# Optimization experiments

Hardware: AMD Instinct MI355X
Metric: run time of the kernel (lower is better)

The kernel has to match this reference:

```python
import jax, jax.numpy as jnp
import numpy as np

DEPTH = 6
N_LEAF = 2 ** DEPTH          # 64
GATE_COUNT = N_LEAF - 1      # 63
B = 1024
GATING_FEATURES = 512
IN_FEATURES = 512
OUT_FEATURES = 512


def setup_inputs() -> dict:
    key = jax.random.key(0)
    k1, k2, k3, k4 = jax.random.split(key, 4)
    x_gating = jax.random.normal(k1, (B, GATING_FEATURES), dtype=jnp.float32)
    x_leaf = jax.random.normal(k2, (B, IN_FEATURES), dtype=jnp.float32)
    # kaiming-normal-ish init scales
    gw = jax.random.normal(k3, (GATING_FEATURES, GATE_COUNT), dtype=jnp.float32) * (1.0 / np.sqrt(GATING_FEATURES))
    gb = jnp.zeros((GATE_COUNT,), dtype=jnp.float32)
    pw = jax.random.normal(k4, (OUT_FEATURES, IN_FEATURES, N_LEAF), dtype=jnp.float32) * (1.0 / np.sqrt(IN_FEATURES))
    pb = jnp.zeros((OUT_FEATURES, N_LEAF), dtype=jnp.float32)
    return {"x_gating": x_gating, "x_leaf": x_leaf, "gw": gw, "gb": gb, "pw": pw, "pb": pb}


def _leaf_probs(x_gating, gw, gb):
    # gatings: (B, gate_count), internal nodes in breadth-first order
    gatings = jax.nn.sigmoid(x_gating @ gw + gb)
    b = gatings.shape[0]
    dens = jnp.ones((b, 1), dtype=gatings.dtype)  # root density
    start = 0
    for d in range(DEPTH):
        n_par = 2 ** d
        g = gatings[:, start:start + n_par]          # (B, n_par)
        # left child (even it+1) gets g, right child gets 1-g, interleaved
        dens = jnp.stack([dens * g, dens * (1.0 - g)], axis=-1).reshape(b, 2 * n_par)
        start += n_par
    return dens  # (B, n_leaf) = leaf densities (last n_leaf node densities)


def reference(x_gating, x_leaf, gw, gb, pw, pb):
    leaf_probs = _leaf_probs(x_gating, gw, gb)              # (B, L)
    # gated projection applied to x_leaf, summed over leaves:
    # equals ((pw @ leaf_probs.T).permute(2,0,1) @ x_leaf[...,None])[...,0]
    result = jnp.einsum('oil,bl,bi->bo', pw, leaf_probs, x_leaf)
    result = result + leaf_probs @ pb.T                     # gated bias (B, O)
    return result
```

## Files before the change

kernel.cpp:

```cpp
#include <hip/hip_runtime.h>
#include <stdint.h>

#define B_SZ   1024
#define GF     512
#define GC     63
#define NLEAF  64
#define IN_F   512
#define OUT_F  512

typedef float f32x4 __attribute__((ext_vector_type(4)));
typedef __fp16 h16x2 __attribute__((ext_vector_type(2)));
typedef __fp16 h16x8 __attribute__((ext_vector_type(8)));
typedef _Float16 f16x2 __attribute__((ext_vector_type(2)));

union HF8 { f16x2 h2[4]; h16x8 v; uint4 u; };

__device__ inline f16x2 pkrtz(float a, float b) {
  union { h16x2 r; f16x2 f; } u;
  u.r = __builtin_amdgcn_cvt_pkrtz(a, b);
  return u.f;
}

__global__ __launch_bounds__(512, 2) void k_leafprobs(
    const float* __restrict__ xg, const float* __restrict__ gw,
    const float* __restrict__ gb, float* __restrict__ p_ws)
{
  __shared__ float xsr[GF];
  __shared__ float part[512];
  __shared__ float gates[GC + 1];
  const int b = blockIdx.x;
  const int t = threadIdx.x;

  xsr[t] = xg[(size_t)b * GF + t];
  __syncthreads();

  const int ks = t >> 6, g = t & 63;
  float acc = 0.f;
  if (g < GC) {
    const float* gp = gw + (size_t)(ks * 64) * GC + g;
    const float* xp = &xsr[ks * 64];
#pragma unroll 8
    for (int k = 0; k < 64; ++k) acc += xp[k] * gp[(size_t)k * GC];
  }
  part[t] = acc;
  __syncthreads();

  if (t < GC) {
    float s = gb[t];
#pragma unroll
    for (int r = 0; r < 8; ++r) s += part[r * 64 + t];
    gates[t] = 1.f / (1.f + expf(-s));
  }
  __syncthreads();

  if (t < NLEAF) {
    float v = 1.f;
    int idx = 0, start = 0;
#pragma unroll
    for (int d = 0; d < 6; ++d) {
      int bit = (t >> (5 - d)) & 1;
      float gg = gates[start + idx];
      v *= bit ? (1.f - gg) : gg;
      idx = 2 * idx + bit;
      start += (1 << d);
    }
    p_ws[(size_t)b * NLEAF + t] = v;
  }
}

#define SK 16
#define KI 32

template <bool ATOMIC>
__global__ __launch_bounds__(256, 2) void k_fused(
    const float* __restrict__ x_leaf,
    const float* __restrict__ p_ws,
    const float* __restrict__ pw,
    float* __restrict__ dst)
{
  __shared__ __align__(16) float         xs[KI][256];
  __shared__ __align__(16) unsigned char bs8[2 * 8192];

  const int tid  = threadIdx.x;
  const int lane = tid & 63;
  const int wid  = tid >> 6;
  const int quad = lane >> 4;
  const int l15  = lane & 15;
  const int l7   = l15 & 7;

  const int bid = blockIdx.x;
  const int nt  = bid & 7;
  const int mt  = (bid >> 3) & 3;
  const int kc  = bid >> 5;

  const int row_m0 = mt * 256;
  const int o0     = nt * 64;
  const int i0     = kc * KI;
  const int wm     = wid * 64;

  {
    const float* src = x_leaf + (size_t)(row_m0 + tid) * IN_F + i0;
#pragma unroll
    for (int q = 0; q < 8; ++q) {
      float4 v = *(const float4*)(src + q * 4);
      xs[q * 4 + 0][tid] = v.x;
      xs[q * 4 + 1][tid] = v.y;
      xs[q * 4 + 2][tid] = v.z;
      xs[q * 4 + 3][tid] = v.w;
    }
  }

  HF8 prh[4][2];
#pragma unroll
  for (int mi = 0; mi < 4; ++mi) {
    const int row = row_m0 + wm + mi * 16 + l15;
#pragma unroll
    for (int ks = 0; ks < 2; ++ks) {
      const f32x4* src = (const f32x4*)(p_ws + (size_t)row * NLEAF + ks * 32 + quad * 8);
      f32x4 lo = src[0], hi = src[1];
      prh[mi][ks].h2[0] = pkrtz(lo.x, lo.y);
      prh[mi][ks].h2[1] = pkrtz(lo.z, lo.w);
      prh[mi][ks].h2[2] = pkrtz(hi.x, hi.y);
      prh[mi][ks].h2[3] = pkrtz(hi.z, hi.w);
    }
  }

  const int br  = tid >> 2;
  const int seg = tid & 3;
  const float* bsrc0 = pw + ((size_t)(o0 + br) * IN_F + i0) * NLEAF + seg * 16;

  const int wsw   = (br & 7) << 4;
  const int woff0 = br * 128 + ((seg * 32) ^ wsw);
  const int woff1 = br * 128 + ((seg * 32 + 16) ^ wsw);
  int coff[2];
#pragma unroll
  for (int ks = 0; ks < 2; ++ks)
    coff[ks] = (ks * 64 + quad * 16) ^ (l7 << 4);
  const int rbase = l15 * 128;

  f32x4 acc[4][4];
#pragma unroll
  for (int mi = 0; mi < 4; ++mi)
#pragma unroll
    for (int ni = 0; ni < 4; ++ni)
      acc[mi][ni] = (f32x4)(0.f);

  float4 rb[4][4];

#define BLOAD(T, SLOT)                                                        \
  {                                                                           \
    const float4* s_ = (const float4*)(bsrc0 + (size_t)(T) * NLEAF);          \
    rb[SLOT][0] = s_[0]; rb[SLOT][1] = s_[1];                                 \
    rb[SLOT][2] = s_[2]; rb[SLOT][3] = s_[3];                                 \
  }

#define BSTAGE(SLOT, BUF)                                                     \
  {                                                                           \
    HF8 c0_, c1_;                                                             \
    float4 a0_ = rb[SLOT][0], a1_ = rb[SLOT][1];                              \
    float4 a2_ = rb[SLOT][2], a3_ = rb[SLOT][3];                              \
    c0_.h2[0] = pkrtz(a0_.x, a0_.y);                                          \
    c0_.h2[1] = pkrtz(a0_.z, a0_.w);                                          \
    c0_.h2[2] = pkrtz(a1_.x, a1_.y);                                          \
    c0_.h2[3] = pkrtz(a1_.z, a1_.w);                                          \
    c1_.h2[0] = pkrtz(a2_.x, a2_.y);                                          \
    c1_.h2[1] = pkrtz(a2_.z, a2_.w);                                          \
    c1_.h2[2] = pkrtz(a3_.x, a3_.y);                                          \
    c1_.h2[3] = pkrtz(a3_.z, a3_.w);                                          \
    *(uint4*)(bs8 + (BUF) * 8192 + woff0) = c0_.u;                            \
    *(uint4*)(bs8 + (BUF) * 8192 + woff1) = c1_.u;                            \
  }

#define BARRIER() asm volatile("s_waitcnt lgkmcnt(0)\n\ts_barrier" ::: "memory")

#define STEP(IT, BUF, SNX)                                                    \
  {                                                                           \
    float xvf[4];                                                             \
    _Float16 xh[4];                                                           \
    _Pragma("unroll")                                                         \
    for (int mi = 0; mi < 4; ++mi) xvf[mi] = xs[(IT)][wm + mi * 16 + l15];    \
    _Pragma("unroll")                                                         \
    for (int mi = 0; mi < 4; ++mi) xh[mi] = (_Float16)xvf[mi];                \
    const unsigned char* bsr_ = bs8 + (BUF) * 8192;                           \
    __builtin_amdgcn_s_setprio(1);                                            \
    _Pragma("unroll")                                                         \
    for (int ks = 0; ks < 2; ++ks) {                                          \
      h16x8 af[4];                                                            \
      _Pragma("unroll")                                                       \
      for (int mi = 0; mi < 4; ++mi) {                                        \
        HF8 t_;                                                               \
        f16x2 xp_; xp_[0] = xh[mi]; xp_[1] = xh[mi];                          \
        _Pragma("unroll")                                                     \
        for (int j = 0; j < 4; ++j) t_.h2[j] = prh[mi][ks].h2[j] * xp_;       \
        af[mi] = t_.v;                                                        \
      }                                                                       \
      _Pragma("unroll")                                                       \
      for (int ni = 0; ni < 4; ++ni) {                                        \
        h16x8 bfr = *(const h16x8*)(bsr_ + ni * 2048 + rbase + coff[ks]);     \
        _Pragma("unroll")                                                     \
        for (int mi = 0; mi < 4; ++mi)                                        \
          acc[mi][ni] = __builtin_amdgcn_mfma_f32_16x16x32_f16(               \
              af[mi], bfr, acc[mi][ni], 0, 0, 0);                             \
      }                                                                       \
    }                                                                         \
    __builtin_amdgcn_s_setprio(0);                                            \
    if ((IT) + 1 < KI) { BSTAGE(SNX, (BUF) ^ 1) }                             \
    if ((IT) + 5 < KI) { BLOAD((IT) + 5, SNX) }                               \
    BARRIER();                                                                \
  }

  BLOAD(0, 0)
  BLOAD(1, 1)
  BLOAD(2, 2)
  BLOAD(3, 3)
  BSTAGE(0, 0)
  BLOAD(4, 0)
  BARRIER();

  for (int itb = 0; itb < KI; itb += 4) {
    STEP(itb + 0, 0, 1)
    STEP(itb + 1, 1, 2)
    STEP(itb + 2, 0, 3)
    STEP(itb + 3, 1, 0)
  }
#undef BLOAD
#undef BSTAGE
#undef BARRIER
#undef STEP

#pragma unroll
  for (int mi = 0; mi < 4; ++mi) {
#pragma unroll
    for (int ni = 0; ni < 4; ++ni) {
      int row = row_m0 + wm + mi * 16 + quad * 4;
      int col = o0 + ni * 16 + l15;
      if (ATOMIC) {
        float* o = dst + (size_t)row * OUT_F + col;
        atomicAdd(o,             acc[mi][ni][0]);
        atomicAdd(o + OUT_F,     acc[mi][ni][1]);
        atomicAdd(o + 2 * OUT_F, acc[mi][ni][2]);
        atomicAdd(o + 3 * OUT_F, acc[mi][ni][3]);
      } else {
        float* o = dst + ((size_t)kc << 19) + (size_t)row * OUT_F + col;
        o[0]         = acc[mi][ni][0];
        o[OUT_F]     = acc[mi][ni][1];
        o[2 * OUT_F] = acc[mi][ni][2];
        o[3 * OUT_F] = acc[mi][ni][3];
      }
    }
  }
}

__global__ __launch_bounds__(256, 4) void k_reduce(
    const float* __restrict__ parts, const float* __restrict__ p_ws,
    const float* __restrict__ pb, float* __restrict__ out, int nparts)
{
  __shared__ float ps_l[2 * NLEAF];
  const int t  = threadIdx.x;
  const int b0 = blockIdx.x * 2;

  if (t < 32)
    ((f32x4*)ps_l)[t] = ((const f32x4*)(p_ws + (size_t)b0 * NLEAF))[t];
  __syncthreads();

  const int row = b0 + (t >> 7);
  const int c0  = (t & 127) * 4;
  const f32x4* ps = (const f32x4*)&ps_l[(t >> 7) * NLEAF];

  f32x4 a;
#pragma unroll
  for (int jo = 0; jo < 4; ++jo) {
    const f32x4* pbo = (const f32x4*)(pb + (size_t)(c0 + jo) * NLEAF);
    f32x4 s = (f32x4)(0.f);
#pragma unroll
    for (int lv = 0; lv < 16; ++lv) s += pbo[lv] * ps[lv];
    a[jo] = s.x + s.y + s.z + s.w;
  }

#pragma unroll 8
  for (int k = 0; k < nparts; ++k)
    a += *(const f32x4*)(parts + ((size_t)k << 19) + (size_t)row * OUT_F + c0);

  *(f32x4*)(out + (size_t)row * OUT_F + c0) = a;
}

extern "C" void kernel_launch(void* const* d_in, const int* in_sizes, int n_in,
                              void* d_out, int out_size, void* d_ws, size_t ws_size,
                              hipStream_t stream) {
  const float* xg = (const float*)d_in[0];
  const float* xl = (const float*)d_in[1];
  const float* gw = (const float*)d_in[2];
  const float* gb = (const float*)d_in[3];
  const float* pw = (const float*)d_in[4];
  const float* pb = (const float*)d_in[5];
  float* out = (float*)d_out;

  const size_t P_BYTES = (size_t)B_SZ * NLEAF * 4;
  const size_t SLICE   = (size_t)B_SZ * OUT_F * 4;

  float* p_ws  = (float*)d_ws;
  float* parts = (float*)((char*)d_ws + P_BYTES);

  k_leafprobs<<<dim3(B_SZ), dim3(512), 0, stream>>>(xg, gw, gb, p_ws);

  if (ws_size >= P_BYTES + SK * SLICE) {
    k_fused<false><<<dim3(512), dim3(256), 0, stream>>>(xl, p_ws, pw, parts);
    k_reduce<<<dim3(512), dim3(256), 0, stream>>>(parts, p_ws, pb, out, SK);
  } else {
    k_reduce<<<dim3(512), dim3(256), 0, stream>>>(parts, p_ws, pb, out, 0);
    k_fused<true><<<dim3(512), dim3(256), 0, stream>>>(xl, p_ws, pw, out);
  }
}
```

Baseline: 167.4 us.

## Load weight fragments directly into registers, dropping LDS staging and per-step barriers

The pw operand for the MFMA is no longer staged through shared memory. Each lane now loads its own B fragment straight from global memory with inline-asm dwordx4 loads, using a one-step register prefetch and explicit vmcnt waits, so the LDS stores, LDS reads and per-iteration barriers go away. The cost is that each wave loads its 64x64 weight tile independently, so the four waves in a block load the same data four times. The prefetch is also shallower than the previous four-slot register ring, so global latency is less hidden.

```diff
diff --git a/kernel.cpp b/kernel.cpp
--- a/kernel.cpp
+++ b/kernel.cpp
@@ -78,15 +78,13 @@
     const float* __restrict__ pw,
     float* __restrict__ dst)
 {
-  __shared__ __align__(16) float         xs[KI][256];
-  __shared__ __align__(16) unsigned char bs8[2 * 8192];
+  __shared__ __align__(16) float xs[KI][256];
 
   const int tid  = threadIdx.x;
   const int lane = tid & 63;
   const int wid  = tid >> 6;
   const int quad = lane >> 4;
   const int l15  = lane & 15;
-  const int l7   = l15 & 7;
 
   const int bid = blockIdx.x;
   const int nt  = bid & 7;
@@ -109,6 +107,7 @@
       xs[q * 4 + 3][tid] = v.w;
     }
   }
+  __syncthreads();
 
   HF8 prh[4][2];
 #pragma unroll
@@ -118,25 +117,17 @@
     for (int ks = 0; ks < 2; ++ks) {
       const f32x4* src = (const f32x4*)(p_ws + (size_t)row * NLEAF + ks * 32 + quad * 8);
       f32x4 lo = src[0], hi = src[1];
-      prh[mi][ks].h2[0] = pkrtz(lo.x, lo.y);
-      prh[mi][ks].h2[1] = pkrtz(lo.z, lo.w);
-      prh[mi][ks].h2[2] = pkrtz(hi.x, hi.y);
-      prh[mi][ks].h2[3] = pkrtz(hi.z, hi.w);
+      prh[mi][ks].h2[0] = pkrtz(lo[0], lo[1]);
+      prh[mi][ks].h2[1] = pkrtz(lo[2], lo[3]);
+      prh[mi][ks].h2[2] = pkrtz(hi[0], hi[1]);
+      prh[mi][ks].h2[3] = pkrtz(hi[2], hi[3]);
     }
   }
 
-  const int br  = tid >> 2;
-  const int seg = tid & 3;
-  const float* bsrc0 = pw + ((size_t)(o0 + br) * IN_F + i0) * NLEAF + seg * 16;
-
-  const int wsw   = (br & 7) << 4;
-  const int woff0 = br * 128 + ((seg * 32) ^ wsw);
-  const int woff1 = br * 128 + ((seg * 32 + 16) ^ wsw);
-  int coff[2];
-#pragma unroll
-  for (int ks = 0; ks < 2; ++ks)
-    coff[ks] = (ks * 64 + quad * 16) ^ (l7 << 4);
-  const int rbase = l15 * 128;
+  const float* p0 = pw + (((size_t)(o0 + l15) * IN_F + i0) * NLEAF + quad * 8);
+  const float* p1 = p0 + (size_t)16 * IN_F * NLEAF;
+  const float* p2 = p0 + (size_t)32 * IN_F * NLEAF;
+  const float* p3 = p0 + (size_t)48 * IN_F * NLEAF;
 
   f32x4 acc[4][4];
 #pragma unroll
@@ -145,35 +136,51 @@
     for (int ni = 0; ni < 4; ++ni)
       acc[mi][ni] = (f32x4)(0.f);
 
-  float4 rb[4][4];
-
-#define BLOAD(T, SLOT)                                                        \
+  f32x4 raw0[4], raw1[4], raw2[4], raw3[4];
+  HF8 fr[2][4];
+
+#define BLOADN(PN, RAW)                                                       \
+  asm volatile(                                                               \
+      "global_load_dwordx4 %0, %4, off\n\t"                                   \
+      "global_load_dwordx4 %1, %4, off offset:16\n\t"                         \
+      "global_load_dwordx4 %2, %4, off offset:128\n\t"                        \
+      "global_load_dwordx4 %3, %4, off offset:144"                            \
+      : "=&v"(RAW[0]), "=&v"(RAW[1]), "=&v"(RAW[2]), "=&v"(RAW[3])            \
+      : "v"(PN) : "memory");
+
+#define BWAITR(RAW, N)                                                        \
+  asm volatile("s_waitcnt vmcnt(" #N ")"                                      \
+               : "+v"(RAW[0]), "+v"(RAW[1]), "+v"(RAW[2]), "+v"(RAW[3])       \
+               ::"memory");                                                   \
+  __builtin_amdgcn_sched_barrier(0);
+
+#define CVTN(RAW, NI)                                                         \
   {                                                                           \
-    const float4* s_ = (const float4*)(bsrc0 + (size_t)(T) * NLEAF);          \
-    rb[SLOT][0] = s_[0]; rb[SLOT][1] = s_[1];                                 \
-    rb[SLOT][2] = s_[2]; rb[SLOT][3] = s_[3];                                 \
-  }
-
-#define BSTAGE(SLOT, BUF)                                                     \
+    fr[0][NI].h2[0] = pkrtz(RAW[0][0], RAW[0][1]);                            \
+    fr[0][NI].h2[1] = pkrtz(RAW[0][2], RAW[0][3]);                            \
+    fr[0][NI].h2[2] = pkrtz(RAW[1][0], RAW[1][1]);                            \
+    fr[0][NI].h2[3] = pkrtz(RAW[1][2], RAW[1][3]);                            \
+    fr[1][NI].h2[0] = pkrtz(RAW[2][0], RAW[2][1]);                            \
+    fr[1][NI].h2[1] = pkrtz(RAW[2][2], RAW[2][3]);                            \
+    fr[1][NI].h2[2] = pkrtz(RAW[3][0], RAW[3][1]);                            \
+    fr[1][NI].h2[3] = pkrtz(RAW[3][2], RAW[3][3]);                            \
+  }
+
+#define BLOADALL()                                                            \
   {                                                                           \
-    HF8 c0_, c1_;                                                             \
-    float4 a0_ = rb[SLOT][0], a1_ = rb[SLOT][1];                              \
-    float4 a2_ = rb[SLOT][2], a3_ = rb[SLOT][3];                              \
-    c0_.h2[0] = pkrtz(a0_.x, a0_.y);                                          \
-    c0_.h2[1] = pkrtz(a0_.z, a0_.w);                                          \
-    c0_.h2[2] = pkrtz(a1_.x, a1_.y);                                          \
-    c0_.h2[3] = pkrtz(a1_.z, a1_.w);                                          \
-    c1_.h2[0] = pkrtz(a2_.x, a2_.y);                                          \
-    c1_.h2[1] = pkrtz(a2_.z, a2_.w);                                          \
-    c1_.h2[2] = pkrtz(a3_.x, a3_.y);                                          \
-    c1_.h2[3] = pkrtz(a3_.z, a3_.w);                                          \
-    *(uint4*)(bs8 + (BUF) * 8192 + woff0) = c0_.u;                            \
-    *(uint4*)(bs8 + (BUF) * 8192 + woff1) = c1_.u;                            \
-  }
-
-#define BARRIER() asm volatile("s_waitcnt lgkmcnt(0)\n\ts_barrier" ::: "memory")
-
-#define STEP(IT, BUF, SNX)                                                    \
+    BLOADN(p0, raw0) BLOADN(p1, raw1) BLOADN(p2, raw2) BLOADN(p3, raw3)       \
+    p0 += NLEAF; p1 += NLEAF; p2 += NLEAF; p3 += NLEAF;                       \
+  }
+
+#define CVTALL()                                                              \
+  {                                                                           \
+    BWAITR(raw0, 12) CVTN(raw0, 0)                                            \
+    BWAITR(raw1, 8)  CVTN(raw1, 1)                                            \
+    BWAITR(raw2, 4)  CVTN(raw2, 2)                                            \
+    BWAITR(raw3, 0)  CVTN(raw3, 3)                                            \
+  }
+
+#define COMPUTE(IT)                                                           \
   {                                                                           \
     float xvf[4];                                                             \
     _Float16 xh[4];                                                           \
@@ -181,7 +188,6 @@
     for (int mi = 0; mi < 4; ++mi) xvf[mi] = xs[(IT)][wm + mi * 16 + l15];    \
     _Pragma("unroll")                                                         \
     for (int mi = 0; mi < 4; ++mi) xh[mi] = (_Float16)xvf[mi];                \
-    const unsigned char* bsr_ = bs8 + (BUF) * 8192;                           \
     __builtin_amdgcn_s_setprio(1);                                            \
     _Pragma("unroll")                                                         \
     for (int ks = 0; ks < 2; ++ks) {                                          \
@@ -196,37 +202,34 @@
       }                                                                       \
       _Pragma("unroll")                                                       \
       for (int ni = 0; ni < 4; ++ni) {                                        \
-        h16x8 bfr = *(const h16x8*)(bsr_ + ni * 2048 + rbase + coff[ks]);     \
         _Pragma("unroll")                                                     \
         for (int mi = 0; mi < 4; ++mi)                                        \
           acc[mi][ni] = __builtin_amdgcn_mfma_f32_16x16x32_f16(               \
-              af[mi], bfr, acc[mi][ni], 0, 0, 0);                             \
+              af[mi], fr[ks][ni].v, acc[mi][ni], 0, 0, 0);                    \
       }                                                                       \
     }                                                                         \
     __builtin_amdgcn_s_setprio(0);                                            \
-    if ((IT) + 1 < KI) { BSTAGE(SNX, (BUF) ^ 1) }                             \
-    if ((IT) + 5 < KI) { BLOAD((IT) + 5, SNX) }                               \
-    BARRIER();                                                                \
-  }
-
-  BLOAD(0, 0)
-  BLOAD(1, 1)
-  BLOAD(2, 2)
-  BLOAD(3, 3)
-  BSTAGE(0, 0)
-  BLOAD(4, 0)
-  BARRIER();
-
-  for (int itb = 0; itb < KI; itb += 4) {
-    STEP(itb + 0, 0, 1)
-    STEP(itb + 1, 1, 2)
-    STEP(itb + 2, 0, 3)
-    STEP(itb + 3, 1, 0)
-  }
-#undef BLOAD
-#undef BSTAGE
-#undef BARRIER
-#undef STEP
+  }
+
+  BLOADALL()
+  CVTALL()
+  BLOADALL()
+
+  for (int it = 0; it < KI - 2; ++it) {
+    COMPUTE(it)
+    CVTALL()
+    BLOADALL()
+  }
+  COMPUTE(KI - 2)
+  CVTALL()
+  COMPUTE(KI - 1)
+
+#undef BLOADN
+#undef BWAITR
+#undef CVTN
+#undef BLOADALL
+#undef CVTALL
+#undef COMPUTE
 
 #pragma unroll
   for (int mi = 0; mi < 4; ++mi) {
@@ -274,7 +277,7 @@
     f32x4 s = (f32x4)(0.f);
 #pragma unroll
     for (int lv = 0; lv < 16; ++lv) s += pbo[lv] * ps[lv];
-    a[jo] = s.x + s.y + s.z + s.w;
+    a[jo] = s[0] + s[1] + s[2] + s[3];
   }
 
 #pragma unroll 8
```

Result: slower. 244.8 us (+46.3%).
